# Kernel tuning notes

Hardware: AMD Instinct MI355X
Metric: run time of the kernel (lower is better)

Reference implementation:

```python
import jax, jax.numpy as jnp
import numpy as np

T, B, D = 1024, 32, 256
TRACE, CTX, OUT = 64, 16, 256


def setup_inputs() -> dict:
    key = jax.random.key(0)
    ks = jax.random.split(key, 12)
    x = jax.random.normal(ks[0], (T, B, D), dtype=jnp.float32)
    start = jax.random.randint(ks[1], (T, B), 0, 2).astype(bool)
    state_re = jnp.zeros((B, TRACE, CTX), dtype=jnp.float32)
    state_im = jnp.zeros((B, TRACE, CTX), dtype=jnp.float32)
    s = 0.02
    w_gate_in = s * jax.random.normal(ks[2], (D, TRACE), dtype=jnp.float32)
    b_gate_in = jnp.zeros((TRACE,), jnp.float32)
    w_pre = s * jax.random.normal(ks[3], (D, TRACE), dtype=jnp.float32)
    b_pre = jnp.zeros((TRACE,), jnp.float32)
    w_z = s * jax.random.normal(ks[4], (2 * TRACE * CTX, OUT), dtype=jnp.float32)
    b_z = jnp.zeros((OUT,), jnp.float32)
    w_gate_out = s * jax.random.normal(ks[5], (D, OUT), dtype=jnp.float32)
    b_gate_out = jnp.zeros((OUT,), jnp.float32)
    w_skip = s * jax.random.normal(ks[6], (D, OUT), dtype=jnp.float32)
    b_skip = jnp.zeros((OUT,), jnp.float32)
    # deterministic FFM params per init_deterministic_a/b
    ffm_a = jnp.linspace(1e-6, 0.5, TRACE).astype(jnp.float32)
    ffm_b = (2 * jnp.pi / jnp.linspace(1.0, 1000.0, CTX)).astype(jnp.float32)
    return dict(x=x, start=start, state_re=state_re, state_im=state_im,
                w_gate_in=w_gate_in, b_gate_in=b_gate_in, w_pre=w_pre, b_pre=b_pre,
                w_z=w_z, b_z=b_z, w_gate_out=w_gate_out, b_gate_out=b_gate_out,
                w_skip=w_skip, b_skip=b_skip, ffm_a=ffm_a, ffm_b=ffm_b)


def _layer_norm(y, eps=1e-6):
    mu = jnp.mean(y, axis=-1, keepdims=True)
    var = jnp.mean(jnp.square(y - mu), axis=-1, keepdims=True)
    return (y - mu) / jnp.sqrt(var + eps)


def _ffm_forward(x, start, state_re, state_im, w_gate_in, b_gate_in, w_pre, b_pre,
                 w_z, b_z, w_gate_out, b_gate_out, w_skip, b_skip, ffm_a, ffm_b):
    Tn, Bn = x.shape[0], x.shape[1]
    # map_to_h
    gate_in = jax.nn.sigmoid(x @ w_gate_in + b_gate_in)           # [T,B,trace]
    gated = (x @ w_pre + b_pre) * gate_in                          # [T,B,trace]
    scan_in = jnp.broadcast_to(gated[..., None], (Tn, Bn, TRACE, CTX)).astype(jnp.complex64)
    # log_gamma decay matrix ab: [1,1,trace,ctx] complex
    a = -jnp.abs(ffm_a).reshape(1, 1, TRACE, 1)
    b = ffm_b.reshape(1, 1, 1, CTX)
    ab = jax.lax.complex(jnp.broadcast_to(a, (1, 1, TRACE, CTX)),
                         jnp.broadcast_to(b, (1, 1, TRACE, CTX)))
    # scan: prepend initial state, reset-aware associative update
    state0 = jax.lax.complex(state_re, state_im)[None]             # [1,B,trace,ctx]
    xs = jnp.concatenate([state0, scan_in], axis=0)                # [T+1,B,trace,ctx]
    st = jnp.concatenate([jnp.zeros((1, Bn, 1, 1), bool),
                          start.reshape(Tn, Bn, 1, 1)], axis=0)    # [T+1,B,1,1]
    ts = jnp.ones((Tn + 1, Bn, 1, 1), dtype=jnp.float32)

    def update(carry, incoming):
        prev_start, s, i = carry
        stt, xx, j = incoming
        keep = jnp.logical_not(stt)
        s = s * keep
        j = j * keep
        s = s * jnp.exp(ab * j) + xx
        return (jnp.logical_or(stt, prev_start), s, j + i)

    _, new_state, _ = jax.lax.associative_scan(update, (st, xs, ts), axis=0)
    state = new_state[1:]                                          # [T,B,trace,ctx]
    # map_from_h
    z_in = jnp.concatenate([jnp.real(state), jnp.imag(state)], axis=-1).reshape(Tn, Bn, -1)
    z = z_in @ w_z + b_z                                           # [T,B,out]
    gate_out = jax.nn.sigmoid(x @ w_gate_out + b_gate_out)
    skip = x @ w_skip + b_skip
    out = _layer_norm(z * gate_out) + skip * (1.0 - gate_out)
    final_state = state[-1]                                        # [B,trace,ctx]
    return final_state, out


def reference(x, start, state_re, state_im, w_gate_in, b_gate_in, w_pre, b_pre,
              w_z, b_z, w_gate_out, b_gate_out, w_skip, b_skip, ffm_a, ffm_b):
    return _ffm_forward(x, start, state_re, state_im, w_gate_in, b_gate_in,
                        w_pre, b_pre, w_z, b_z, w_gate_out, b_gate_out,
                        w_skip, b_skip, ffm_a, ffm_b)
```

## Files before the change

kernel.cpp:

```cpp
#include <hip/hip_runtime.h>
#include <hip/hip_bf16.h>

#define T_DIM 1024
#define B_DIM 32
#define D_DIM 256
#define TRACE 64
#define CTX 16
#define OUT_DIM 256
#define TB (T_DIM * B_DIM)
#define KZ (2 * TRACE * CTX)
#define NP 640
#define NCH 16
#define CHL 64

typedef short short8 __attribute__((ext_vector_type(8)));
typedef float floatx4 __attribute__((ext_vector_type(4)));
typedef unsigned short ushortx4 __attribute__((ext_vector_type(4)));

__device__ __forceinline__ float bf2f(unsigned short u) {
  return __uint_as_float((unsigned int)u << 16);
}
__device__ __forceinline__ float sigm(float v) {
  return 1.f / (1.f + expf(-v));
}
__device__ __forceinline__ void gload_lds16(const void* g, void* l) {
  __builtin_amdgcn_global_load_lds(
      (const __attribute__((address_space(1))) void*)g,
      (__attribute__((address_space(3))) void*)l, 16, 0, 0);
}

__global__ __launch_bounds__(256) void k_prep_all(
    const unsigned char* __restrict__ s, int* __restrict__ startw,
    const float* __restrict__ wz, __hip_bfloat16* __restrict__ wzt,
    const float* __restrict__ wgi, const float* __restrict__ bgi,
    const float* __restrict__ wpr, const float* __restrict__ bpr,
    const float* __restrict__ wgo, const float* __restrict__ bgo,
    const float* __restrict__ wsk, const float* __restrict__ bsk,
    __hip_bfloat16* __restrict__ wcat, float* __restrict__ bcat,
    const float* __restrict__ x, __hip_bfloat16* __restrict__ xb) {
  const int bid = blockIdx.x;
  const int tid = threadIdx.x;
  if (bid < 4096) {
    size_t i = ((size_t)bid * 256 + tid) * 8;
    float4 a = *reinterpret_cast<const float4*>(x + i);
    float4 b = *reinterpret_cast<const float4*>(x + i + 4);
    unsigned short u[8];
    u[0] = __bfloat16_as_ushort(__float2bfloat16(a.x));
    u[1] = __bfloat16_as_ushort(__float2bfloat16(a.y));
    u[2] = __bfloat16_as_ushort(__float2bfloat16(a.z));
    u[3] = __bfloat16_as_ushort(__float2bfloat16(a.w));
    u[4] = __bfloat16_as_ushort(__float2bfloat16(b.x));
    u[5] = __bfloat16_as_ushort(__float2bfloat16(b.y));
    u[6] = __bfloat16_as_ushort(__float2bfloat16(b.z));
    u[7] = __bfloat16_as_ushort(__float2bfloat16(b.w));
    *reinterpret_cast<uint4*>(xb + i) = *reinterpret_cast<uint4*>(u);
    return;
  }
  if (bid < 4128) {
    unsigned o1 = 0, o3 = 0, o4 = 0;
    for (int i = tid; i < 2048; i += 256) {
      uint4 wv = reinterpret_cast<const uint4*>(s)[i];
      unsigned allw = wv.x | wv.y | wv.z | wv.w;
      o1 |= allw & 0x0000FF00u;
      o3 |= allw & 0xFF000000u;
      o4 |= (wv.y | wv.w) & 0x000000FFu;
    }
    __shared__ unsigned s1, s3, s4;
    if (tid == 0) { s1 = 0; s3 = 0; s4 = 0; }
    __syncthreads();
    if (o1) atomicOr(&s1, 1u);
    if (o3) atomicOr(&s3, 1u);
    if (o4) atomicOr(&s4, 1u);
    __syncthreads();
    int f = s1 ? 1 : (s3 ? 2 : (s4 ? 0 : 3));
    int base = (bid - 4096) * 1024 + tid * 4;
    int4 v;
    if (f == 1) {
      uchar4 b4 = reinterpret_cast<const uchar4*>(s)[base >> 2];
      v = make_int4(b4.x != 0, b4.y != 0, b4.z != 0, b4.w != 0);
    } else if (f == 2) {
      float4 fv = reinterpret_cast<const float4*>(s)[base >> 2];
      v = make_int4(fv.x != 0.f, fv.y != 0.f, fv.z != 0.f, fv.w != 0.f);
    } else if (f == 3) {
      const long long* p = reinterpret_cast<const long long*>(s);
      v = make_int4(p[base] != 0, p[base + 1] != 0,
                    p[base + 2] != 0, p[base + 3] != 0);
    } else {
      int4 iv = reinterpret_cast<const int4*>(s)[base >> 2];
      v = make_int4(iv.x != 0, iv.y != 0, iv.z != 0, iv.w != 0);
    }
    reinterpret_cast<int4*>(startw)[base >> 2] = v;
    return;
  }
  if (bid < 4256) {
    const int t = bid - 4128;
    const int tk = t & 31;
    const int tn = t >> 5;
    const int k0 = tk * 64, n0 = tn * 64;
    __shared__ float sm[64][65];
    for (int i = tid; i < 4096; i += 256) {
      int r = i >> 6, c = i & 63;
      sm[r][c] = wz[(size_t)(k0 + r) * 256 + n0 + c];
    }
    __syncthreads();
    for (int i = tid; i < 4096; i += 256) {
      int r = i >> 6, c = i & 63;
      int src = (c & 0x20) | ((c & 1) << 4) | ((c >> 1) & 15);
      wzt[(size_t)(n0 + r) * 2048 + k0 + c] = __float2bfloat16(sm[src][r]);
    }
    return;
  }
  const int n = bid - 4256, k = tid;
  float v, bv;
  if (n < 64)        { v = wgi[k * 64 + n];          bv = bgi[n]; }
  else if (n < 128)  { v = wpr[k * 64 + (n - 64)];   bv = bpr[n - 64]; }
  else if (n < 384)  { v = wgo[k * 256 + (n - 128)]; bv = bgo[n - 128]; }
  else               { v = wsk[k * 256 + (n - 384)]; bv = bsk[n - 384]; }
  wcat[(size_t)n * 256 + k] = __float2bfloat16(v);
  if (k == 0) bcat[n] = bv;
}

__global__ __launch_bounds__(256) void k_gemm_xproj(
    const __hip_bfloat16* __restrict__ A, const __hip_bfloat16* __restrict__ Bm,
    const float* __restrict__ bias, __hip_bfloat16* __restrict__ C) {
  int wg = (blockIdx.x & 7) * 160 + (blockIdx.x >> 3);
  const int n0 = (wg % 5) * 128;
  const int r0 = (wg / 5) * 128;
  const int tid = threadIdx.x;
  const int l = tid & 63;
  const int wid = tid >> 6;
  const int wr = wid >> 1;
  const int wc = wid & 1;

  __shared__ __align__(16) char ldsA[16384];
  __shared__ __align__(16) char ldsB[16384];

  floatx4 acc[4][4];
#pragma unroll
  for (int m = 0; m < 4; ++m)
#pragma unroll
    for (int n = 0; n < 4; ++n) acc[m][n] = (floatx4)0.f;

  int aoff[4][2], boff[4][2];
#pragma unroll
  for (int m = 0; m < 4; ++m) {
    int row = wr * 64 + m * 16 + (l & 15);
#pragma unroll
    for (int ks = 0; ks < 2; ++ks) {
      int byte = row * 128 + ks * 64 + (l >> 4) * 16;
      aoff[m][ks] = byte ^ ((row & 7) << 4);
    }
    int col = wc * 64 + m * 16 + (l & 15);
#pragma unroll
    for (int ks = 0; ks < 2; ++ks) {
      int byte = col * 128 + ks * 64 + (l >> 4) * 16;
      boff[m][ks] = byte ^ ((col & 7) << 4);
    }
  }

  for (int kt = 0; kt < 256; kt += 64) {
#pragma unroll
    for (int i = 0; i < 4; ++i) {
      int c = tid + i * 256;
      int row = c >> 3;
      int kgs = (c & 7) ^ (row & 7);
      gload_lds16(A + (size_t)(r0 + row) * 256 + kt + kgs * 8,
                  ldsA + i * 4096 + wid * 1024);
      gload_lds16(Bm + (size_t)(n0 + row) * 256 + kt + kgs * 8,
                  ldsB + i * 4096 + wid * 1024);
    }
    __syncthreads();
#pragma unroll
    for (int ks = 0; ks < 2; ++ks) {
      short8 a[4], b[4];
#pragma unroll
      for (int m = 0; m < 4; ++m)
        a[m] = *reinterpret_cast<const short8*>(ldsA + aoff[m][ks]);
#pragma unroll
      for (int n = 0; n < 4; ++n)
        b[n] = *reinterpret_cast<const short8*>(ldsB + boff[n][ks]);
#pragma unroll
      for (int m = 0; m < 4; ++m)
#pragma unroll
        for (int n = 0; n < 4; ++n)
          acc[m][n] = __builtin_amdgcn_mfma_f32_16x16x32_bf16(
              a[m], b[n], acc[m][n], 0, 0, 0);
    }
    __syncthreads();
  }

#pragma unroll
  for (int m = 0; m < 4; ++m) {
#pragma unroll
    for (int n = 0; n < 4; ++n) {
      int gc = n0 + wc * 64 + n * 16 + (l & 15);
      float bzv = bias[gc];
      bool dosig = (gc < 64) || (gc >= 128 && gc < 384);
#pragma unroll
      for (int j = 0; j < 4; ++j) {
        int gr = r0 + wr * 64 + m * 16 + (l >> 4) * 4 + j;
        float v = acc[m][n][j] + bzv;
        if (dosig) v = sigm(v);
        C[(size_t)gr * NP + gc] = __float2bfloat16(v);
      }
    }
  }
}

__global__ __launch_bounds__(256, 2) void k_zgemm_ln(
    const __hip_bfloat16* __restrict__ zin, const __hip_bfloat16* __restrict__ wzt,
    const float* __restrict__ bz, const __hip_bfloat16* __restrict__ proj,
    float* __restrict__ out) {
  const int r0 = blockIdx.x * 64;
  const int tid = threadIdx.x;
  const int l = tid & 63;
  const int w = tid >> 6;

  __shared__ __align__(16) char lds[81920];
  float* red1 = (float*)lds;
  float* red2 = (float*)(lds + 1024);

  floatx4 acc[4][4];
#pragma unroll
  for (int m = 0; m < 4; ++m)
#pragma unroll
    for (int n = 0; n < 4; ++n) acc[m][n] = (floatx4)0.f;

  int aoff[4][2], boff[4][2];
#pragma unroll
  for (int m = 0; m < 4; ++m) {
    int row = m * 16 + (l & 15);
#pragma unroll
    for (int ks = 0; ks < 2; ++ks) {
      int byte = row * 128 + ks * 64 + (l >> 4) * 16;
      aoff[m][ks] = byte ^ ((row & 7) << 4);
    }
  }
#pragma unroll
  for (int n = 0; n < 4; ++n) {
    int col = w * 64 + n * 16 + (l & 15);
#pragma unroll
    for (int ks = 0; ks < 2; ++ks) {
      int byte = col * 128 + ks * 64 + (l >> 4) * 16;
      boff[n][ks] = byte ^ ((col & 7) << 4);
    }
  }

  auto STAGE = [&](int kt, int sel) {
    char* pA = lds + (sel ? 8192 : 0);
    char* pB = lds + 16384 + (sel ? 32768 : 0);
#pragma unroll
    for (int i = 0; i < 2; ++i) {
      int c = tid + i * 256;
      int row = c >> 3;
      int kgs = (c & 7) ^ (row & 7);
      gload_lds16(zin + (size_t)(r0 + row) * KZ + kt + kgs * 8,
                  pA + i * 4096 + w * 1024);
    }
#pragma unroll
    for (int i = 0; i < 8; ++i) {
      int c = tid + i * 256;
      int row = c >> 3;
      int kgs = (c & 7) ^ (row & 7);
      gload_lds16(wzt + (size_t)row * KZ + kt + kgs * 8,
                  pB + i * 4096 + w * 1024);
    }
  };
  auto COMPUTE = [&](int sel) {
    const char* pA = lds + (sel ? 8192 : 0);
    const char* pB = lds + 16384 + (sel ? 32768 : 0);
#pragma unroll
    for (int ks = 0; ks < 2; ++ks) {
      short8 a[4], b[4];
#pragma unroll
      for (int m = 0; m < 4; ++m)
        a[m] = *reinterpret_cast<const short8*>(pA + aoff[m][ks]);
#pragma unroll
      for (int n = 0; n < 4; ++n)
        b[n] = *reinterpret_cast<const short8*>(pB + boff[n][ks]);
#pragma unroll
      for (int m = 0; m < 4; ++m)
#pragma unroll
        for (int n = 0; n < 4; ++n)
          acc[m][n] = __builtin_amdgcn_mfma_f32_16x16x32_bf16(
              a[m], b[n], acc[m][n], 0, 0, 0);
    }
  };

  STAGE(0, 0);
  asm volatile("s_waitcnt vmcnt(0)" ::: "memory");
  __builtin_amdgcn_s_barrier();
  for (int t = 0; t < 31; ++t) {
    STAGE((t + 1) * 64, (t + 1) & 1);
    COMPUTE(t & 1);
    asm volatile("s_waitcnt vmcnt(0)" ::: "memory");
    __builtin_amdgcn_s_barrier();
  }
  COMPUTE(1);

  float bzv[4];
#pragma unroll
  for (int n = 0; n < 4; ++n) bzv[n] = bz[w * 64 + n * 16 + (l & 15)];

  float q[4][4][4];
#pragma unroll
  for (int m = 0; m < 4; ++m) {
#pragma unroll
    for (int j = 0; j < 4; ++j) {
      int row = m * 16 + (l >> 4) * 4 + j;
      const __hip_bfloat16* prow = proj + (size_t)(r0 + row) * NP;
      float s1 = 0.f, s2 = 0.f;
#pragma unroll
      for (int n = 0; n < 4; ++n) {
        int col = w * 64 + n * 16 + (l & 15);
        float go = __bfloat162float(prow[128 + col]);
        float ps = __bfloat162float(prow[384 + col]);
        float y = (acc[m][n][j] + bzv[n]) * go;
        acc[m][n][j] = y;
        q[m][n][j] = ps * (1.f - go);
        s1 += y;
        s2 += y * y;
      }
#pragma unroll
      for (int off = 8; off > 0; off >>= 1) {
        s1 += __shfl_xor(s1, off);
        s2 += __shfl_xor(s2, off);
      }
      if ((l & 15) == 0) { red1[row * 4 + w] = s1; red2[row * 4 + w] = s2; }
    }
  }
  __syncthreads();

#pragma unroll
  for (int m = 0; m < 4; ++m) {
#pragma unroll
    for (int j = 0; j < 4; ++j) {
      int row = m * 16 + (l >> 4) * 4 + j;
      int gr = r0 + row;
      float t1 = red1[row * 4 + 0] + red1[row * 4 + 1] +
                 red1[row * 4 + 2] + red1[row * 4 + 3];
      float t2 = red2[row * 4 + 0] + red2[row * 4 + 1] +
                 red2[row * 4 + 2] + red2[row * 4 + 3];
      float mu = t1 * (1.f / 256.f);
      float var = t2 * (1.f / 256.f) - mu * mu;
      float rs = rsqrtf(var + 1e-6f);
#pragma unroll
      for (int n = 0; n < 4; ++n) {
        int col = w * 64 + n * 16 + (l & 15);
        out[(size_t)gr * 256 + col] = (acc[m][n][j] - mu) * rs + q[m][n][j];
      }
    }
  }
}

__global__ __launch_bounds__(64) void k_scan_a(
    const __hip_bfloat16* __restrict__ proj, const int* __restrict__ startw,
    const float* __restrict__ ffm_a, const float* __restrict__ ffm_b,
    float2* __restrict__ carry, int* __restrict__ rstflag) {
  const int c  = blockIdx.x >> 9;
  const int bb = (blockIdx.x >> 4) & 31;
  const int tg = blockIdx.x & 15;
  const int tid = threadIdx.x;
  const int tl = tid >> 4, cx = tid & 15;
  const int trace = tg * 4 + tl;
  const int t0 = c * CHL;
  __shared__ float gs[CHL * 4];
  __shared__ int ss[CHL];
  for (int t = tid; t < CHL; t += 64) {
    size_t base = ((size_t)(t0 + t) * B_DIM + bb) * NP + tg * 4;
    ushortx4 pg4 = *reinterpret_cast<const ushortx4*>(proj + base);
    ushortx4 pp4 = *reinterpret_cast<const ushortx4*>(proj + base + 64);
    float4 o;
    o.x = bf2f(pp4[0]) * bf2f(pg4[0]);
    o.y = bf2f(pp4[1]) * bf2f(pg4[1]);
    o.z = bf2f(pp4[2]) * bf2f(pg4[2]);
    o.w = bf2f(pp4[3]) * bf2f(pg4[3]);
    *reinterpret_cast<float4*>(&gs[t * 4]) = o;
    ss[t] = startw[(t0 + t) * B_DIM + bb];
  }
  __syncthreads();

  int any = __any(ss[tid] != 0);
  if (tid == 0 && tg == 0) rstflag[c * B_DIM + bb] = any;

  float decay = expf(-fabsf(ffm_a[trace]));
  float th = ffm_b[cx];
  float cr = decay * cosf(th);
  float ci = decay * sinf(th);
  float sr = 0.f, si = 0.f;
  for (int t = 0; t < CHL; ++t) {
    float g = gs[t * 4 + tl];
    int rst = ss[t];
    float nr = fmaf(sr, cr, fmaf(-si, ci, g));
    float ni = fmaf(sr, ci, si * cr);
    sr = rst ? g : nr;
    si = rst ? 0.f : ni;
  }
  carry[((size_t)(c * B_DIM + bb) * TRACE + trace) * CTX + cx] =
      make_float2(sr, si);
}

__global__ __launch_bounds__(64) void k_scan_c(
    const __hip_bfloat16* __restrict__ proj, const int* __restrict__ startw,
    const float* __restrict__ state_re, const float* __restrict__ state_im,
    const float* __restrict__ ffm_a, const float* __restrict__ ffm_b,
    const float2* __restrict__ carry, const int* __restrict__ rstflag,
    __hip_bfloat16* __restrict__ zin, float* __restrict__ fstate) {
  const int c  = blockIdx.x >> 9;
  const int bb = (blockIdx.x >> 4) & 31;
  const int tg = blockIdx.x & 15;
  const int tid = threadIdx.x;
  const int tl = tid >> 4, cx = tid & 15;
  const int trace = tg * 4 + tl;
  const int t0 = c * CHL;
  __shared__ float gs[CHL * 4];
  __shared__ int ss[CHL];
  for (int t = tid; t < CHL; t += 64) {
    size_t base = ((size_t)(t0 + t) * B_DIM + bb) * NP + tg * 4;
    ushortx4 pg4 = *reinterpret_cast<const ushortx4*>(proj + base);
    ushortx4 pp4 = *reinterpret_cast<const ushortx4*>(proj + base + 64);
    float4 o;
    o.x = bf2f(pp4[0]) * bf2f(pg4[0]);
    o.y = bf2f(pp4[1]) * bf2f(pg4[1]);
    o.z = bf2f(pp4[2]) * bf2f(pg4[2]);
    o.w = bf2f(pp4[3]) * bf2f(pg4[3]);
    *reinterpret_cast<float4*>(&gs[t * 4]) = o;
    ss[t] = startw[(t0 + t) * B_DIM + bb];
  }
  __syncthreads();

  float decay = expf(-fabsf(ffm_a[trace]));
  float th = ffm_b[cx];
  float cr = decay * cosf(th);
  float ci = decay * sinf(th);

  float pr = cr, pi = ci;
#pragma unroll
  for (int q = 0; q < 6; ++q) {
    float nr = pr * pr - pi * pi;
    float ni = 2.f * pr * pi;
    pr = nr; pi = ni;
  }

  const int chain = (bb * TRACE + trace) * CTX + cx;
  float sr = state_re[chain];
  float si = state_im[chain];
  for (int j = 0; j < c; ++j) {
    float2 cj = carry[((size_t)(j * B_DIM + bb) * TRACE + trace) * CTX + cx];
    if (rstflag[j * B_DIM + bb]) {
      sr = cj.x; si = cj.y;
    } else {
      float nsr = fmaf(pr, sr, fmaf(-pi, si, cj.x));
      float nsi = fmaf(pr, si, fmaf(pi, sr, cj.y));
      sr = nsr; si = nsi;
    }
  }

  const size_t zbase = (size_t)trace * 32 + cx * 2;
  for (int t = 0; t < CHL; ++t) {
    float g = gs[t * 4 + tl];
    int rst = ss[t];
    float nr = fmaf(sr, cr, fmaf(-si, ci, g));
    float ni = fmaf(sr, ci, si * cr);
    sr = rst ? g : nr;
    si = rst ? 0.f : ni;
    unsigned int u = (unsigned int)__bfloat16_as_ushort(__float2bfloat16(sr)) |
                     ((unsigned int)__bfloat16_as_ushort(__float2bfloat16(si)) << 16);
    *reinterpret_cast<unsigned int*>(
        zin + ((size_t)(t0 + t) * B_DIM + bb) * KZ + zbase) = u;
  }
  if (c == NCH - 1) fstate[chain] = sr;
}

extern "C" void kernel_launch(void* const* d_in, const int* in_sizes, int n_in,
                              void* d_out, int out_size, void* d_ws, size_t ws_size,
                              hipStream_t stream) {
  const float* x         = (const float*)d_in[0];
  const unsigned char* start_raw = (const unsigned char*)d_in[1];
  const float* state_re  = (const float*)d_in[2];
  const float* state_im  = (const float*)d_in[3];
  const float* w_gate_in = (const float*)d_in[4];
  const float* b_gate_in = (const float*)d_in[5];
  const float* w_pre     = (const float*)d_in[6];
  const float* b_pre     = (const float*)d_in[7];
  const float* w_z       = (const float*)d_in[8];
  const float* b_z       = (const float*)d_in[9];
  const float* w_gate_out= (const float*)d_in[10];
  const float* b_gate_out= (const float*)d_in[11];
  const float* w_skip    = (const float*)d_in[12];
  const float* b_skip    = (const float*)d_in[13];
  const float* ffm_a     = (const float*)d_in[14];
  const float* ffm_b     = (const float*)d_in[15];

  char* ws = (char*)d_ws;
  int* startw   = (int*)(ws + 4096);
  int* rstflag  = (int*)(ws + (132 << 10));
  float* bcat   = (float*)(ws + (160 << 10));
  __hip_bfloat16* wcat =
      (__hip_bfloat16*)(ws + (256 << 10));
  __hip_bfloat16* wzt =
      (__hip_bfloat16*)(ws + ((size_t)1 << 20));
  float2* carry = (float2*)(ws + ((size_t)2 << 20));
  __hip_bfloat16* proj =
      (__hip_bfloat16*)(ws + ((size_t)6 << 20));
  __hip_bfloat16* xb =
      (__hip_bfloat16*)(ws + ((size_t)46 << 20));
  __hip_bfloat16* zin =
      (__hip_bfloat16*)(ws + ((size_t)62 << 20));

  float* fstate = (float*)d_out;
  float* out    = (float*)d_out + B_DIM * TRACE * CTX;

  k_prep_all<<<4896, 256, 0, stream>>>(
      start_raw, startw, w_z, wzt,
      w_gate_in, b_gate_in, w_pre, b_pre,
      w_gate_out, b_gate_out, w_skip, b_skip,
      wcat, bcat, x, xb);
  k_gemm_xproj<<<1280, 256, 0, stream>>>(xb, wcat, bcat, proj);
  k_scan_a<<<(NCH - 1) * B_DIM * 16, 64, 0, stream>>>(
      proj, startw, ffm_a, ffm_b, carry, rstflag);
  k_scan_c<<<NCH * B_DIM * 16, 64, 0, stream>>>(
      proj, startw, state_re, state_im, ffm_a, ffm_b, carry, rstflag,
      zin, fstate);
  k_zgemm_ln<<<TB / 64, 256, 0, stream>>>(zin, wzt, b_z, proj, out);
}
```

Baseline: 146.2 us.

## Read Wz operand directly from global memory instead of LDS staging in zgemm

The z-GEMM+layernorm kernel no longer stages the weight (B) tiles through shared memory. Each wave loads its B fragments straight from global memory, relying on L2/cache reuse across blocks. This shrinks LDS from 80KB to about 18KB, and launch bounds are raised to 3 blocks per CU for more occupancy. The risk is that per-wave global loads of B sit on the MFMA critical path with no prefetch, and waves in different blocks re-read the same weights, which adds latency and cache traffic.

Result: slower. 221.7 us (+51.7%).

```diff
diff --git a/kernel.cpp b/kernel.cpp
--- a/kernel.cpp
+++ b/kernel.cpp
@@ -207,7 +207,7 @@
   }
 }
 
-__global__ __launch_bounds__(256, 2) void k_zgemm_ln(
+__global__ __launch_bounds__(256, 3) void k_zgemm_ln(
     const __hip_bfloat16* __restrict__ zin, const __hip_bfloat16* __restrict__ wzt,
     const float* __restrict__ bz, const __hip_bfloat16* __restrict__ proj,
     float* __restrict__ out) {
@@ -216,9 +216,8 @@
   const int l = tid & 63;
   const int w = tid >> 6;
 
-  __shared__ __align__(16) char lds[81920];
-  float* red1 = (float*)lds;
-  float* red2 = (float*)(lds + 1024);
+  __shared__ __align__(16) char lds[16384];
+  __shared__ float red1[256], red2[256];
 
   floatx4 acc[4][4];
 #pragma unroll
@@ -226,7 +225,7 @@
 #pragma unroll
     for (int n = 0; n < 4; ++n) acc[m][n] = (floatx4)0.f;
 
-  int aoff[4][2], boff[4][2];
+  int aoff[4][2];
 #pragma unroll
   for (int m = 0; m < 4; ++m) {
     int row = m * 16 + (l & 15);
@@ -236,19 +235,11 @@
       aoff[m][ks] = byte ^ ((row & 7) << 4);
     }
   }
-#pragma unroll
-  for (int n = 0; n < 4; ++n) {
-    int col = w * 64 + n * 16 + (l & 15);
-#pragma unroll
-    for (int ks = 0; ks < 2; ++ks) {
-      int byte = col * 128 + ks * 64 + (l >> 4) * 16;
-      boff[n][ks] = byte ^ ((col & 7) << 4);
-    }
-  }
+  const __hip_bfloat16* bbase =
+      wzt + (size_t)(w * 64 + (l & 15)) * KZ + (l >> 4) * 8;
 
   auto STAGE = [&](int kt, int sel) {
     char* pA = lds + (sel ? 8192 : 0);
-    char* pB = lds + 16384 + (sel ? 32768 : 0);
 #pragma unroll
     for (int i = 0; i < 2; ++i) {
       int c = tid + i * 256;
@@ -257,18 +248,9 @@
       gload_lds16(zin + (size_t)(r0 + row) * KZ + kt + kgs * 8,
                   pA + i * 4096 + w * 1024);
     }
-#pragma unroll
-    for (int i = 0; i < 8; ++i) {
-      int c = tid + i * 256;
-      int row = c >> 3;
-      int kgs = (c & 7) ^ (row & 7);
-      gload_lds16(wzt + (size_t)row * KZ + kt + kgs * 8,
-                  pB + i * 4096 + w * 1024);
-    }
   };
-  auto COMPUTE = [&](int sel) {
+  auto COMPUTE = [&](int sel, int kt) {
     const char* pA = lds + (sel ? 8192 : 0);
-    const char* pB = lds + 16384 + (sel ? 32768 : 0);
 #pragma unroll
     for (int ks = 0; ks < 2; ++ks) {
       short8 a[4], b[4];
@@ -277,7 +259,7 @@
         a[m] = *reinterpret_cast<const short8*>(pA + aoff[m][ks]);
 #pragma unroll
       for (int n = 0; n < 4; ++n)
-        b[n] = *reinterpret_cast<const short8*>(pB + boff[n][ks]);
+        b[n] = *reinterpret_cast<const short8*>(bbase + n * 16 * KZ + kt + ks * 32);
 #pragma unroll
       for (int m = 0; m < 4; ++m)
 #pragma unroll
@@ -292,11 +274,11 @@
   __builtin_amdgcn_s_barrier();
   for (int t = 0; t < 31; ++t) {
     STAGE((t + 1) * 64, (t + 1) & 1);
-    COMPUTE(t & 1);
+    COMPUTE(t & 1, t * 64);
     asm volatile("s_waitcnt vmcnt(0)" ::: "memory");
     __builtin_amdgcn_s_barrier();
   }
-  COMPUTE(1);
+  COMPUTE(1, 31 * 64);
 
   float bzv[4];
 #pragma unroll
```
